# Kernel tuning notes

Hardware: AMD Instinct MI355X
Metric: run time of the kernel (lower is better)

The kernel has to match this reference:

```python
import jax, jax.numpy as jnp
import numpy as np

N, G, E, F, H = 100000, 32768, 1000000, 128, 128

def _mlp(x, w1, b1, w2, b2):
    # Linear -> SiLU -> Linear
    return jax.nn.silu(x @ w1 + b1) @ w2 + b2

def setup_inputs() -> dict:
    key = jax.random.key(0)
    ks = jax.random.split(key, 24)
    s = 0.02
    p = lambda k, shp: (jax.random.normal(k, shp, dtype=jnp.float32) * s)
    inp = {
        "node_features": jax.random.normal(ks[0], (N, F), dtype=jnp.float32),
        "node_pos": jax.random.normal(ks[1], (N, 3), dtype=jnp.float32),
        "grid_pos": jax.random.normal(ks[2], (G, 3), dtype=jnp.float32),
        "edge_index": jax.random.randint(ks[3], (2, E), 0, G, dtype=jnp.int64),
        "orientations": jax.random.normal(ks[4], (N, 3, 3), dtype=jnp.float32),
        # node_model
        "nw1": p(ks[5], (F, H)), "nb1": p(ks[6], (H,)),
        "nw2": p(ks[7], (H, H)), "nb2": p(ks[8], (H,)),
        # edge_model
        "ew1": p(ks[9], (6, H)), "eb1": p(ks[10], (H,)),
        "ew2": p(ks[11], (H, H)), "eb2": p(ks[12], (H,)),
        # message_model
        "mw1": p(ks[13], (2 * H, H)), "mb1": p(ks[14], (H,)),
        "mw2": p(ks[15], (H, H)), "mb2": p(ks[16], (H,)),
        # update_model
        "uw1": p(ks[17], (H, H)), "ub1": p(ks[18], (H,)),
        "uw2": p(ks[19], (H, H)), "ub2": p(ks[20], (H,)),
    }
    return inp

def reference(node_features, node_pos, grid_pos, edge_index, orientations,
              nw1, nb1, nw2, nb2, ew1, eb1, ew2, eb2,
              mw1, mb1, mw2, mb2, uw1, ub1, uw2, ub2):
    src, tgt = edge_index[0], edge_index[1]
    # node MLP on all points [N, H]
    node_h = _mlp(node_features, nw1, nb1, nw2, nb2)
    # per-edge geometry
    pos_src = node_pos[src]                     # [E, 3]
    rel_pos = grid_pos[tgt] - pos_src           # [E, 3]
    # bmm(rel_pos[e,1,3], orientations[src][e,3,3]) -> [E, 3]
    rot = jnp.einsum("ej,ejk->ek", rel_pos, orientations[src])
    edge_attr = jnp.concatenate([pos_src, rot], axis=-1)       # [E, 6]
    edge_h = _mlp(edge_attr, ew1, eb1, ew2, eb2)               # [E, H]
    msg_in = jnp.concatenate([node_h[src], edge_h], axis=-1)   # [E, 2H]
    msg = _mlp(msg_in, mw1, mb1, mw2, mb2)                     # [E, H]
    # scatter-mean to grid
    num_grid = grid_pos.shape[0]
    sums = jax.ops.segment_sum(msg, tgt, num_segments=num_grid)             # [G, H]
    counts = jax.ops.segment_sum(jnp.ones((msg.shape[0],), msg.dtype), tgt,
                                 num_segments=num_grid)
    grid_feat = sums / jnp.clip(counts, 1.0)[:, None]
    return _mlp(grid_feat, uw1, ub1, uw2, ub2)
```

## Files before the change

kernel.cpp:

```cpp
#include <hip/hip_runtime.h>

#define P 136

typedef __attribute__((ext_vector_type(8))) short short8;
typedef __attribute__((ext_vector_type(4))) float f32x4;

__device__ __forceinline__ unsigned short f2bf(float f) {
  union { float f; unsigned u; } v; v.f = f;
  unsigned u = v.u + 0x7fffu + ((v.u >> 16) & 1u);
  return (unsigned short)(u >> 16);
}
__device__ __forceinline__ float bf2f(unsigned short h) {
  union { unsigned u; float f; } v; v.u = ((unsigned)h) << 16;
  return v.f;
}
__device__ __forceinline__ unsigned pack2bf(float x, float y) {
  union { float f; unsigned u; } a, b; a.f = x; b.f = y;
  return __builtin_amdgcn_perm(b.u + 0x8000u, a.u + 0x8000u, 0x07060302u);
}
__device__ __forceinline__ float silu_f(float x) {
  float e = __expf(-x);
  return x * __builtin_amdgcn_rcpf(1.0f + e);
}

__device__ __forceinline__ void load_A128(const unsigned short* __restrict__ W,
                                          int m0w, int l16, int q, short8 a[2][4]) {
#pragma unroll
  for (int rt = 0; rt < 2; ++rt)
#pragma unroll
    for (int kt = 0; kt < 4; ++kt)
      a[rt][kt] = *(const short8*)&W[(m0w + rt * 16 + l16) * 128 + kt * 32 + q * 8];
}

template <int CT, bool INIT>
__device__ __forceinline__ void gemm_T(const short8 a[2][4],
                                       const unsigned short* sB,
                                       int l16, int q, f32x4 acc[2][CT]) {
  const f32x4 Z = (f32x4){0.f, 0.f, 0.f, 0.f};
#pragma unroll
  for (int kt = 0; kt < 4; ++kt)
#pragma unroll
    for (int ct = 0; ct < CT; ++ct) {
      short8 b = *(const short8*)&sB[(ct * 16 + l16) * P + kt * 32 + q * 8];
      f32x4 c0 = (INIT && kt == 0) ? Z : acc[0][ct];
      f32x4 c1 = (INIT && kt == 0) ? Z : acc[1][ct];
      acc[0][ct] = __builtin_amdgcn_mfma_f32_16x16x32_bf16(a[0][kt], b, c0, 0, 0, 0);
      acc[1][ct] = __builtin_amdgcn_mfma_f32_16x16x32_bf16(a[1][kt], b, c1, 0, 0, 0);
    }
}

template <bool SILU, int CT>
__device__ __forceinline__ void epilogue_T(const f32x4 acc[2][CT], const float* bias,
                                           unsigned short* sOut, int m0w, int l16,
                                           int q) {
#pragma unroll
  for (int rt = 0; rt < 2; ++rt) {
    int f0 = m0w + rt * 16 + q * 4;
    float4 bv = *(const float4*)&bias[f0];
#pragma unroll
    for (int ct = 0; ct < CT; ++ct) {
      float v0 = acc[rt][ct][0] + bv.x, v1 = acc[rt][ct][1] + bv.y;
      float v2 = acc[rt][ct][2] + bv.z, v3 = acc[rt][ct][3] + bv.w;
      if (SILU) { v0 = silu_f(v0); v1 = silu_f(v1); v2 = silu_f(v2); v3 = silu_f(v3); }
      uint2 w; w.x = pack2bf(v0, v1); w.y = pack2bf(v2, v3);
      *(uint2*)&sOut[(ct * 16 + l16) * P + f0] = w;
    }
  }
}

__global__ __launch_bounds__(256) void fold_hist_kernel(
    const float* __restrict__ nw1, const float* __restrict__ nw2,
    const float* __restrict__ nb2, const float* __restrict__ ew2,
    const float* __restrict__ eb2, const float* __restrict__ mw1,
    const float* __restrict__ mb1, const float* __restrict__ mw2,
    const float* __restrict__ uw1, const float* __restrict__ uw2,
    const float* __restrict__ ew1,
    unsigned short* __restrict__ nw1t, unsigned short* __restrict__ wnt,
    unsigned short* __restrict__ wct, unsigned short* __restrict__ mw2t,
    unsigned short* __restrict__ uw1t, unsigned short* __restrict__ uw2t,
    unsigned short* __restrict__ ew1t8,
    float* __restrict__ bn, float* __restrict__ bc,
    const int* __restrict__ eidx, int* __restrict__ hist, int E) {
  if (blockIdx.x >= 64) {
    int e0 = (blockIdx.x - 64) * 4096 + threadIdx.x * 16;
    if (e0 + 15 < E && (E & 3) == 0) {
      int4 t0 = *(const int4*)&eidx[E + e0];
      int4 t1 = *(const int4*)&eidx[E + e0 + 4];
      int4 t2 = *(const int4*)&eidx[E + e0 + 8];
      int4 t3 = *(const int4*)&eidx[E + e0 + 12];
      atomicAdd(&hist[t0.x], 1); atomicAdd(&hist[t0.y], 1);
      atomicAdd(&hist[t0.z], 1); atomicAdd(&hist[t0.w], 1);
      atomicAdd(&hist[t1.x], 1); atomicAdd(&hist[t1.y], 1);
      atomicAdd(&hist[t1.z], 1); atomicAdd(&hist[t1.w], 1);
      atomicAdd(&hist[t2.x], 1); atomicAdd(&hist[t2.y], 1);
      atomicAdd(&hist[t2.z], 1); atomicAdd(&hist[t2.w], 1);
      atomicAdd(&hist[t3.x], 1); atomicAdd(&hist[t3.y], 1);
      atomicAdd(&hist[t3.z], 1); atomicAdd(&hist[t3.w], 1);
    } else {
#pragma unroll
      for (int k = 0; k < 16; ++k) {
        int e = e0 + k;
        if (e < E) atomicAdd(&hist[eidx[E + e]], 1);
      }
    }
    return;
  }
  int b = blockIdx.x * 2 + (threadIdx.x >> 7);
  int t = threadIdx.x & 127;
  float accn = 0.f, accc = 0.f;
  for (int j = 0; j < 128; ++j) {
    accn += nw2[t * 128 + j] * mw1[j * 128 + b];
    accc += ew2[t * 128 + j] * mw1[(128 + j) * 128 + b];
  }
  wnt[b * 128 + t] = f2bf(accn);
  wct[b * 128 + t] = f2bf(accc);
  nw1t[b * 128 + t] = f2bf(nw1[t * 128 + b]);
  mw2t[b * 128 + t] = f2bf(mw2[t * 128 + b]);
  uw1t[b * 128 + t] = f2bf(uw1[t * 128 + b]);
  uw2t[b * 128 + t] = f2bf(uw2[t * 128 + b]);
  if (t < 8) ew1t8[b * 8 + t] = (t < 6) ? f2bf(ew1[t * 128 + b]) : (unsigned short)0;
  if (b == 0) {
    float sn = 0.f, sc = 0.f;
    for (int j = 0; j < 128; ++j) {
      sn += nb2[j] * mw1[j * 128 + t];
      sc += eb2[j] * mw1[(128 + j) * 128 + t];
    }
    bn[t] = sn;
    bc[t] = mb1[t] + sc;
  }
}

__global__ __launch_bounds__(1024) void scan_kernel(const int* __restrict__ hist,
                                                    int* __restrict__ cursor, int G) {
  __shared__ int s[1024];
  int tid = threadIdx.x;
  int per = (G + 1023) >> 10;
  int b0 = tid * per;
  bool vec = ((per & 3) == 0) && ((G & 3) == 0) && (b0 + per <= G);
  int sum = 0;
  if (vec) {
    for (int i = 0; i < per; i += 4) {
      int4 h = *(const int4*)&hist[b0 + i];
      sum += h.x + h.y + h.z + h.w;
    }
  } else {
    for (int i = 0; i < per; ++i)
      if (b0 + i < G) sum += hist[b0 + i];
  }
  s[tid] = sum;
  __syncthreads();
  for (int off = 1; off < 1024; off <<= 1) {
    int v = (tid >= off) ? s[tid - off] : 0;
    __syncthreads();
    s[tid] += v;
    __syncthreads();
  }
  int run = s[tid] - sum;
  if (vec) {
    for (int i = 0; i < per; i += 4) {
      int4 h = *(const int4*)&hist[b0 + i];
      int4 c;
      c.x = run;
      c.y = c.x + h.x;
      c.z = c.y + h.y;
      c.w = c.z + h.z;
      *(int4*)&cursor[b0 + i] = c;
      run = c.w + h.w;
    }
  } else {
    for (int i = 0; i < per; ++i)
      if (b0 + i < G) {
        cursor[b0 + i] = run;
        run += hist[b0 + i];
      }
  }
}

__global__ __launch_bounds__(256, 3) void scatter_node_kernel(
    const int* __restrict__ eidx, int* __restrict__ cursor,
    int2* __restrict__ st, int E, int nNode,
    const float* __restrict__ x, const float* __restrict__ nb1,
    const unsigned short* __restrict__ nw1t, const unsigned short* __restrict__ wnt,
    const float* __restrict__ bn, unsigned short* __restrict__ node_pre, int N) {
  __shared__ __align__(16) unsigned short s_x[128 * P];
  __shared__ __align__(16) float s_b1[128];
  __shared__ __align__(16) float s_bn[128];

  if (blockIdx.x >= (unsigned)nNode) {
    int e0 = (blockIdx.x - nNode) * 4096 + threadIdx.x * 16;
    if (e0 + 15 < E && (E & 3) == 0) {
      int4 sv[4], tv[4];
#pragma unroll
      for (int g = 0; g < 4; ++g) {
        sv[g] = *(const int4*)&eidx[e0 + g * 4];
        tv[g] = *(const int4*)&eidx[E + e0 + g * 4];
      }
      int pos[16];
#pragma unroll
      for (int g = 0; g < 4; ++g) {
        pos[g * 4 + 0] = atomicAdd(&cursor[tv[g].x], 1);
        pos[g * 4 + 1] = atomicAdd(&cursor[tv[g].y], 1);
        pos[g * 4 + 2] = atomicAdd(&cursor[tv[g].z], 1);
        pos[g * 4 + 3] = atomicAdd(&cursor[tv[g].w], 1);
      }
#pragma unroll
      for (int g = 0; g < 4; ++g) {
        st[pos[g * 4 + 0]] = make_int2(sv[g].x, tv[g].x);
        st[pos[g * 4 + 1]] = make_int2(sv[g].y, tv[g].y);
        st[pos[g * 4 + 2]] = make_int2(sv[g].z, tv[g].z);
        st[pos[g * 4 + 3]] = make_int2(sv[g].w, tv[g].w);
      }
    } else {
#pragma unroll
      for (int k = 0; k < 16; ++k) {
        int e = e0 + k;
        if (e < E) {
          int tg = eidx[E + e];
          int p = atomicAdd(&cursor[tg], 1);
          st[p] = make_int2(eidx[e], tg);
        }
      }
    }
    return;
  }

  int tid = threadIdx.x;
  long base = (long)blockIdx.x * 128;

#pragma unroll
  for (int i = 0; i < 16; ++i) {
    int flat = tid + i * 256;
    int row = flat >> 5;
    int c4 = (flat & 31) << 2;
    float4 v = make_float4(0.f, 0.f, 0.f, 0.f);
    if (base + row < N) v = *(const float4*)&x[(base + row) * 128 + c4];
    uint2 w; w.x = pack2bf(v.x, v.y); w.y = pack2bf(v.z, v.w);
    *(uint2*)&s_x[row * P + c4] = w;
  }
  if (tid < 128) { s_b1[tid] = nb1[tid]; s_bn[tid] = bn[tid]; }
  __syncthreads();

  int wave = tid >> 6, lane = tid & 63;
  int q = lane >> 4, l16 = lane & 15;
  int m0w = wave * 32;

  short8 a1[2][4];
  load_A128(nw1t, m0w, l16, q, a1);
  f32x4 acc[2][8];
  gemm_T<8, true>(a1, s_x, l16, q, acc);
  __syncthreads();
  epilogue_T<true, 8>(acc, s_b1, s_x, m0w, l16, q);
  __syncthreads();

  short8 a2[2][4];
  load_A128(wnt, m0w, l16, q, a2);
  gemm_T<8, true>(a2, s_x, l16, q, acc);

#pragma unroll
  for (int rt = 0; rt < 2; ++rt) {
    int f0 = m0w + rt * 16 + q * 4;
    float4 bv = *(const float4*)&s_bn[f0];
#pragma unroll
    for (int ct = 0; ct < 8; ++ct) {
      long n = base + ct * 16 + l16;
      if (n < N) {
        uint2 w;
        w.x = pack2bf(acc[rt][ct][0] + bv.x, acc[rt][ct][1] + bv.y);
        w.y = pack2bf(acc[rt][ct][2] + bv.z, acc[rt][ct][3] + bv.w);
        *(uint2*)&node_pre[n * 128 + f0] = w;
      }
    }
  }
}

__global__ __launch_bounds__(256, 4) void edge_kernel(
    const int2* __restrict__ st_sorted, const float* __restrict__ node_pos,
    const float* __restrict__ grid_pos, const float* __restrict__ ori,
    const unsigned short* __restrict__ ew1t8, const float* __restrict__ eb1,
    const unsigned short* __restrict__ wct, const float* __restrict__ bc,
    const unsigned short* __restrict__ node_pre, float* __restrict__ sums, int E) {
  __shared__ __align__(16) unsigned short s_h[128 * P];
  __shared__ int s_src[128];
  __shared__ int s_tgt[128];
  __shared__ __align__(16) float s_eb1[128];
  __shared__ __align__(16) float s_bc[128];

  int tid = threadIdx.x;
  int base = blockIdx.x * 128;

  if (tid < 128) {
    s_eb1[tid] = eb1[tid];
    s_bc[tid] = bc[tid];
    int eg = base + tid;
    int s = 0, tg = -1;
    float a0 = 0.f, a1 = 0.f, a2 = 0.f, a3 = 0.f, a4 = 0.f, a5 = 0.f;
    if (eg < E) {
      int2 st = st_sorted[eg];
      s = st.x; tg = st.y;
      float2 p01 = *(const float2*)&node_pos[s * 3];
      float pz = node_pos[s * 3 + 2];
      float2 g01 = *(const float2*)&grid_pos[tg * 3];
      float gz = grid_pos[tg * 3 + 2];
      float4 o0 = *(const float4*)&ori[(long)s * 9];
      float4 o1 = *(const float4*)&ori[(long)s * 9 + 4];
      float o8 = ori[(long)s * 9 + 8];
      float rx = g01.x - p01.x, ry = g01.y - p01.y, rz = gz - pz;
      a0 = p01.x; a1 = p01.y; a2 = pz;
      a3 = rx * o0.x + ry * o0.w + rz * o1.z;
      a4 = rx * o0.y + ry * o1.x + rz * o1.w;
      a5 = rx * o0.z + ry * o1.y + rz * o8;
    }
    s_src[tid] = s;
    s_tgt[tid] = tg;
    uint4 w0;
    w0.x = pack2bf(a0, a1); w0.y = pack2bf(a2, a3); w0.z = pack2bf(a4, a5); w0.w = 0u;
    *(uint4*)&s_h[tid * P] = w0;
  }

  int wave = tid >> 6, lane = tid & 63;
  int q = lane >> 4, l16 = lane & 15;
  int m0w = wave * 32;
  short8 z8 = (short8){0, 0, 0, 0, 0, 0, 0, 0};
  const f32x4 Z = (f32x4){0.f, 0.f, 0.f, 0.f};

  short8 ae0 = z8, ae1 = z8;
  if (q == 0) {
    ae0 = *(const short8*)&ew1t8[(m0w + l16) * 8];
    ae1 = *(const short8*)&ew1t8[(m0w + 16 + l16) * 8];
  }

  __syncthreads();

  short8 pre[8];
#pragma unroll
  for (int ct = 0; ct < 8; ++ct) {
    long srow = (long)s_src[ct * 16 + l16] * 128;
    pre[ct] = *(const short8*)&node_pre[srow + m0w + q * 8];
  }

  f32x4 acc[2][8];
#pragma unroll
  for (int ct = 0; ct < 8; ++ct) {
    short8 b = z8;
    if (q == 0) b = *(const short8*)&s_h[(ct * 16 + l16) * P];
    acc[0][ct] = __builtin_amdgcn_mfma_f32_16x16x32_bf16(ae0, b, Z, 0, 0, 0);
    acc[1][ct] = __builtin_amdgcn_mfma_f32_16x16x32_bf16(ae1, b, Z, 0, 0, 0);
  }
  __syncthreads();

  epilogue_T<true, 8>(acc, s_eb1, s_h, m0w, l16, q);

  short8 awc[2][4];
  load_A128(wct, m0w, l16, q, awc);

  __syncthreads();

  short8 aI_lo, aI_hi;
#pragma unroll
  for (int j = 0; j < 8; ++j) {
    aI_lo[j] = ((q * 8 + j) == l16) ? (short)0x3F80 : (short)0;
    aI_hi[j] = ((q * 8 + j) == (l16 + 16)) ? (short)0x3F80 : (short)0;
  }
#pragma unroll
  for (int ct = 0; ct < 8; ++ct) {
    acc[0][ct] = __builtin_amdgcn_mfma_f32_16x16x32_bf16(aI_lo, pre[ct], Z, 0, 0, 0);
    acc[1][ct] = __builtin_amdgcn_mfma_f32_16x16x32_bf16(aI_hi, pre[ct], Z, 0, 0, 0);
  }

  gemm_T<8, false>(awc, s_h, l16, q, acc);
  __syncthreads();

  epilogue_T<true, 8>(acc, s_bc, s_h, m0w, l16, q);
  __syncthreads();

  {
    int cq = tid & 31;
    int chunk = tid >> 5;
    int c0 = cq * 4;
    int row0 = chunk * 16;
    float v0 = 0.f, v1 = 0.f, v2 = 0.f, v3 = 0.f;
    int cur = s_tgt[row0];
    for (int r = 0; r < 16; ++r) {
      int row = row0 + r;
      int tg = s_tgt[row];
      if (tg != cur) {
        if (cur >= 0) {
          atomicAdd(&sums[(long)cur * 128 + c0], v0);
          atomicAdd(&sums[(long)cur * 128 + c0 + 1], v1);
          atomicAdd(&sums[(long)cur * 128 + c0 + 2], v2);
          atomicAdd(&sums[(long)cur * 128 + c0 + 3], v3);
        }
        v0 = 0.f; v1 = 0.f; v2 = 0.f; v3 = 0.f; cur = tg;
      }
      uint2 w = *(const uint2*)&s_h[row * P + c0];
      v0 += bf2f((unsigned short)w.x);
      v1 += bf2f((unsigned short)(w.x >> 16));
      v2 += bf2f((unsigned short)w.y);
      v3 += bf2f((unsigned short)(w.y >> 16));
    }
    if (cur >= 0) {
      atomicAdd(&sums[(long)cur * 128 + c0], v0);
      atomicAdd(&sums[(long)cur * 128 + c0 + 1], v1);
      atomicAdd(&sums[(long)cur * 128 + c0 + 2], v2);
      atomicAdd(&sums[(long)cur * 128 + c0 + 3], v3);
    }
  }
}

__global__ __launch_bounds__(256, 3) void grid_kernel(
    const float* __restrict__ sums, const int* __restrict__ hist,
    const float* __restrict__ mb2, const float* __restrict__ ub1,
    const float* __restrict__ ub2, const unsigned short* __restrict__ mw2t,
    const unsigned short* __restrict__ uw1t, const unsigned short* __restrict__ uw2t,
    float* __restrict__ out, int G) {
  __shared__ __align__(16) unsigned short s_x[32 * P];
  __shared__ __align__(16) float s_bm[128];
  __shared__ __align__(16) float s_b1[128];
  __shared__ __align__(16) float s_b2[128];
  int tid = threadIdx.x;
  long base = (long)blockIdx.x * 32;

#pragma unroll
  for (int i = 0; i < 4; ++i) {
    int flat = tid + i * 256;
    int row = flat >> 5;
    int c4 = (flat & 31) << 2;
    float4 v = make_float4(0.f, 0.f, 0.f, 0.f);
    float inv = 1.f;
    if (base + row < G) {
      v = *(const float4*)&sums[(base + row) * 128 + c4];
      int c = hist[base + row];
      inv = __builtin_amdgcn_rcpf((float)(c < 1 ? 1 : c));
    }
    uint2 w; w.x = pack2bf(v.x * inv, v.y * inv); w.y = pack2bf(v.z * inv, v.w * inv);
    *(uint2*)&s_x[row * P + c4] = w;
  }
  if (tid < 128) { s_bm[tid] = mb2[tid]; s_b1[tid] = ub1[tid]; s_b2[tid] = ub2[tid]; }
  __syncthreads();

  int wave = tid >> 6, lane = tid & 63;
  int q = lane >> 4, l16 = lane & 15;
  int m0w = wave * 32;

  f32x4 acc[2][2];
  short8 aw[2][4];

  load_A128(mw2t, m0w, l16, q, aw);
  gemm_T<2, true>(aw, s_x, l16, q, acc);
  __syncthreads();
  epilogue_T<false, 2>(acc, s_bm, s_x, m0w, l16, q);
  __syncthreads();

  load_A128(uw1t, m0w, l16, q, aw);
  gemm_T<2, true>(aw, s_x, l16, q, acc);
  __syncthreads();
  epilogue_T<true, 2>(acc, s_b1, s_x, m0w, l16, q);
  __syncthreads();

  load_A128(uw2t, m0w, l16, q, aw);
  gemm_T<2, true>(aw, s_x, l16, q, acc);

#pragma unroll
  for (int rt = 0; rt < 2; ++rt) {
    int f0 = m0w + rt * 16 + q * 4;
    float4 bv = *(const float4*)&s_b2[f0];
#pragma unroll
    for (int ct = 0; ct < 2; ++ct) {
      long g = base + ct * 16 + l16;
      if (g < G) {
        float4 o = make_float4(acc[rt][ct][0] + bv.x, acc[rt][ct][1] + bv.y,
                               acc[rt][ct][2] + bv.z, acc[rt][ct][3] + bv.w);
        *(float4*)&out[g * 128 + f0] = o;
      }
    }
  }
}

extern "C" void kernel_launch(void* const* d_in, const int* in_sizes, int n_in,
                              void* d_out, int out_size, void* d_ws, size_t ws_size,
                              hipStream_t stream) {
  const float* x    = (const float*)d_in[0];
  const float* npos = (const float*)d_in[1];
  const float* gpos = (const float*)d_in[2];
  const int*   eidx = (const int*)d_in[3];
  const float* ori  = (const float*)d_in[4];
  const float* nw1 = (const float*)d_in[5];
  const float* nb1 = (const float*)d_in[6];
  const float* nw2 = (const float*)d_in[7];
  const float* nb2 = (const float*)d_in[8];
  const float* ew1 = (const float*)d_in[9];
  const float* eb1 = (const float*)d_in[10];
  const float* ew2 = (const float*)d_in[11];
  const float* eb2 = (const float*)d_in[12];
  const float* mw1 = (const float*)d_in[13];
  const float* mb1 = (const float*)d_in[14];
  const float* mw2 = (const float*)d_in[15];
  const float* mb2 = (const float*)d_in[16];
  const float* uw1 = (const float*)d_in[17];
  const float* ub1 = (const float*)d_in[18];
  const float* uw2 = (const float*)d_in[19];
  const float* ub2 = (const float*)d_in[20];

  int N = in_sizes[0] / 128;
  int G = in_sizes[2] / 3;
  int E = in_sizes[3] / 2;

  char* ws = (char*)d_ws;
  size_t off = 0;
  float* sums = (float*)(ws + off);            off += (size_t)G * 128 * 4;
  int* hist = (int*)(ws + off);                off += (size_t)G * 4;
  int* cursor = (int*)(ws + off);              off += (size_t)G * 4;
  unsigned short* node_pre = (unsigned short*)(ws + off); off += (size_t)N * 128 * 2;
  off = (off + 255) & ~(size_t)255;
  unsigned short* w_nw1t = (unsigned short*)(ws + off); off += 128 * 128 * 2;
  unsigned short* w_wnt  = (unsigned short*)(ws + off); off += 128 * 128 * 2;
  unsigned short* w_wct  = (unsigned short*)(ws + off); off += 128 * 128 * 2;
  unsigned short* w_mw2t = (unsigned short*)(ws + off); off += 128 * 128 * 2;
  unsigned short* w_uw1t = (unsigned short*)(ws + off); off += 128 * 128 * 2;
  unsigned short* w_uw2t = (unsigned short*)(ws + off); off += 128 * 128 * 2;
  unsigned short* w_ew1t8 = (unsigned short*)(ws + off); off += 128 * 8 * 2;
  float* bn = (float*)(ws + off); off += 128 * 4;
  float* bc = (float*)(ws + off); off += 128 * 4;

  int2* st_sorted = (int2*)d_out;

  int nScat = (E + 4095) / 4096;
  int nNode = (N + 127) / 128;
  int nHist = (E + 4095) / 4096;

  hipMemsetAsync(sums, 0, ((size_t)G * 128 + G) * 4, stream);

  fold_hist_kernel<<<64 + nHist, 256, 0, stream>>>(
      nw1, nw2, nb2, ew2, eb2, mw1, mb1, mw2, uw1, uw2, ew1,
      w_nw1t, w_wnt, w_wct, w_mw2t, w_uw1t, w_uw2t, w_ew1t8, bn, bc,
      eidx, hist, E);
  scan_kernel<<<1, 1024, 0, stream>>>(hist, cursor, G);
  scatter_node_kernel<<<nNode + nScat, 256, 0, stream>>>(
      eidx, cursor, st_sorted, E, nNode,
      x, nb1, w_nw1t, w_wnt, bn, node_pre, N);
  edge_kernel<<<(E + 127) / 128, 256, 0, stream>>>(st_sorted, npos, gpos, ori,
                                                   w_ew1t8, eb1, w_wct, bc,
                                                   node_pre, sums, E);
  grid_kernel<<<(G + 31) / 32, 256, 0, stream>>>(sums, hist, mb2, ub1, ub2,
                                                 w_mw2t, w_uw1t, w_uw2t,
                                                 (float*)d_out, G);
}
```

Measured before the change: 465.4 us.

## Fold biases into MFMA accumulator init and rework edge scatter partitioning

Bias vectors are now loaded into registers and used as the initial MFMA accumulator, so the separate bias adds in every epilogue disappear. The edge kernel's launch bounds go from 4 to 3 blocks per SM, loosening register pressure. The segment-scatter phase now has each thread handle 2 columns over 32 rows instead of 4 columns over 16 rows, halving the atomic flushes per run boundary but lengthening each thread's serial loop.

```diff
diff --git a/kernel.cpp b/kernel.cpp
--- a/kernel.cpp
+++ b/kernel.cpp
@@ -32,35 +32,48 @@
       a[rt][kt] = *(const short8*)&W[(m0w + rt * 16 + l16) * 128 + kt * 32 + q * 8];
 }
 
-template <int CT, bool INIT>
-__device__ __forceinline__ void gemm_T(const short8 a[2][4],
-                                       const unsigned short* sB,
-                                       int l16, int q, f32x4 acc[2][CT]) {
-  const f32x4 Z = (f32x4){0.f, 0.f, 0.f, 0.f};
+template <int CT>
+__device__ __forceinline__ void gemm_T_init(const short8 a[2][4],
+                                            const unsigned short* sB,
+                                            int l16, int q, f32x4 acc[2][CT],
+                                            f32x4 c0i, f32x4 c1i) {
 #pragma unroll
   for (int kt = 0; kt < 4; ++kt)
 #pragma unroll
     for (int ct = 0; ct < CT; ++ct) {
       short8 b = *(const short8*)&sB[(ct * 16 + l16) * P + kt * 32 + q * 8];
-      f32x4 c0 = (INIT && kt == 0) ? Z : acc[0][ct];
-      f32x4 c1 = (INIT && kt == 0) ? Z : acc[1][ct];
+      f32x4 c0 = (kt == 0) ? c0i : acc[0][ct];
+      f32x4 c1 = (kt == 0) ? c1i : acc[1][ct];
       acc[0][ct] = __builtin_amdgcn_mfma_f32_16x16x32_bf16(a[0][kt], b, c0, 0, 0, 0);
       acc[1][ct] = __builtin_amdgcn_mfma_f32_16x16x32_bf16(a[1][kt], b, c1, 0, 0, 0);
     }
 }
 
+template <int CT>
+__device__ __forceinline__ void gemm_T_acc(const short8 a[2][4],
+                                           const unsigned short* sB,
+                                           int l16, int q, f32x4 acc[2][CT]) {
+#pragma unroll
+  for (int kt = 0; kt < 4; ++kt)
+#pragma unroll
+    for (int ct = 0; ct < CT; ++ct) {
+      short8 b = *(const short8*)&sB[(ct * 16 + l16) * P + kt * 32 + q * 8];
+      acc[0][ct] = __builtin_amdgcn_mfma_f32_16x16x32_bf16(a[0][kt], b, acc[0][ct], 0, 0, 0);
+      acc[1][ct] = __builtin_amdgcn_mfma_f32_16x16x32_bf16(a[1][kt], b, acc[1][ct], 0, 0, 0);
+    }
+}
+
 template <bool SILU, int CT>
-__device__ __forceinline__ void epilogue_T(const f32x4 acc[2][CT], const float* bias,
-                                           unsigned short* sOut, int m0w, int l16,
-                                           int q) {
+__device__ __forceinline__ void epilogue_nb(const f32x4 acc[2][CT],
+                                            unsigned short* sOut, int m0w, int l16,
+                                            int q) {
 #pragma unroll
   for (int rt = 0; rt < 2; ++rt) {
     int f0 = m0w + rt * 16 + q * 4;
-    float4 bv = *(const float4*)&bias[f0];
 #pragma unroll
     for (int ct = 0; ct < CT; ++ct) {
-      float v0 = acc[rt][ct][0] + bv.x, v1 = acc[rt][ct][1] + bv.y;
-      float v2 = acc[rt][ct][2] + bv.z, v3 = acc[rt][ct][3] + bv.w;
+      float v0 = acc[rt][ct][0], v1 = acc[rt][ct][1];
+      float v2 = acc[rt][ct][2], v3 = acc[rt][ct][3];
       if (SILU) { v0 = silu_f(v0); v1 = silu_f(v1); v2 = silu_f(v2); v3 = silu_f(v3); }
       uint2 w; w.x = pack2bf(v0, v1); w.y = pack2bf(v2, v3);
       *(uint2*)&sOut[(ct * 16 + l16) * P + f0] = w;
@@ -244,36 +257,40 @@
   int q = lane >> 4, l16 = lane & 15;
   int m0w = wave * 32;
 
+  f32x4 b1_0 = *(const f32x4*)&s_b1[m0w + q * 4];
+  f32x4 b1_1 = *(const f32x4*)&s_b1[m0w + 16 + q * 4];
+
   short8 a1[2][4];
   load_A128(nw1t, m0w, l16, q, a1);
   f32x4 acc[2][8];
-  gemm_T<8, true>(a1, s_x, l16, q, acc);
-  __syncthreads();
-  epilogue_T<true, 8>(acc, s_b1, s_x, m0w, l16, q);
-  __syncthreads();
-
+  gemm_T_init<8>(a1, s_x, l16, q, acc, b1_0, b1_1);
+  __syncthreads();
+  epilogue_nb<true, 8>(acc, s_x, m0w, l16, q);
+  __syncthreads();
+
+  f32x4 bn_0 = *(const f32x4*)&s_bn[m0w + q * 4];
+  f32x4 bn_1 = *(const f32x4*)&s_bn[m0w + 16 + q * 4];
   short8 a2[2][4];
   load_A128(wnt, m0w, l16, q, a2);
-  gemm_T<8, true>(a2, s_x, l16, q, acc);
+  gemm_T_init<8>(a2, s_x, l16, q, acc, bn_0, bn_1);
 
 #pragma unroll
   for (int rt = 0; rt < 2; ++rt) {
     int f0 = m0w + rt * 16 + q * 4;
-    float4 bv = *(const float4*)&s_bn[f0];
 #pragma unroll
     for (int ct = 0; ct < 8; ++ct) {
       long n = base + ct * 16 + l16;
       if (n < N) {
         uint2 w;
-        w.x = pack2bf(acc[rt][ct][0] + bv.x, acc[rt][ct][1] + bv.y);
-        w.y = pack2bf(acc[rt][ct][2] + bv.z, acc[rt][ct][3] + bv.w);
+        w.x = pack2bf(acc[rt][ct][0], acc[rt][ct][1]);
+        w.y = pack2bf(acc[rt][ct][2], acc[rt][ct][3]);
         *(uint2*)&node_pre[n * 128 + f0] = w;
       }
     }
   }
 }
 
-__global__ __launch_bounds__(256, 4) void edge_kernel(
+__global__ __launch_bounds__(256, 3) void edge_kernel(
     const int2* __restrict__ st_sorted, const float* __restrict__ node_pos,
     const float* __restrict__ grid_pos, const float* __restrict__ ori,
     const unsigned short* __restrict__ ew1t8, const float* __restrict__ eb1,
@@ -321,7 +338,6 @@
   int q = lane >> 4, l16 = lane & 15;
   int m0w = wave * 32;
   short8 z8 = (short8){0, 0, 0, 0, 0, 0, 0, 0};
-  const f32x4 Z = (f32x4){0.f, 0.f, 0.f, 0.f};
 
   short8 ae0 = z8, ae1 = z8;
   if (q == 0) {
@@ -338,23 +354,28 @@
     pre[ct] = *(const short8*)&node_pre[srow + m0w + q * 8];
   }
 
+  f32x4 be0 = *(const f32x4*)&s_eb1[m0w + q * 4];
+  f32x4 be1 = *(const f32x4*)&s_eb1[m0w + 16 + q * 4];
+
   f32x4 acc[2][8];
 #pragma unroll
   for (int ct = 0; ct < 8; ++ct) {
     short8 b = z8;
     if (q == 0) b = *(const short8*)&s_h[(ct * 16 + l16) * P];
-    acc[0][ct] = __builtin_amdgcn_mfma_f32_16x16x32_bf16(ae0, b, Z, 0, 0, 0);
-    acc[1][ct] = __builtin_amdgcn_mfma_f32_16x16x32_bf16(ae1, b, Z, 0, 0, 0);
-  }
-  __syncthreads();
-
-  epilogue_T<true, 8>(acc, s_eb1, s_h, m0w, l16, q);
+    acc[0][ct] = __builtin_amdgcn_mfma_f32_16x16x32_bf16(ae0, b, be0, 0, 0, 0);
+    acc[1][ct] = __builtin_amdgcn_mfma_f32_16x16x32_bf16(ae1, b, be1, 0, 0, 0);
+  }
+  __syncthreads();
+
+  epilogue_nb<true, 8>(acc, s_h, m0w, l16, q);
 
   short8 awc[2][4];
   load_A128(wct, m0w, l16, q, awc);
 
   __syncthreads();
 
+  f32x4 bc0 = *(const f32x4*)&s_bc[m0w + q * 4];
+  f32x4 bc1 = *(const f32x4*)&s_bc[m0w + 16 + q * 4];
   short8 aI_lo, aI_hi;
 #pragma unroll
   for (int j = 0; j < 8; ++j) {
@@ -363,46 +384,40 @@
   }
 #pragma unroll
   for (int ct = 0; ct < 8; ++ct) {
-    acc[0][ct] = __builtin_amdgcn_mfma_f32_16x16x32_bf16(aI_lo, pre[ct], Z, 0, 0, 0);
-    acc[1][ct] = __builtin_amdgcn_mfma_f32_16x16x32_bf16(aI_hi, pre[ct], Z, 0, 0, 0);
-  }
-
-  gemm_T<8, false>(awc, s_h, l16, q, acc);
-  __syncthreads();
-
-  epilogue_T<true, 8>(acc, s_bc, s_h, m0w, l16, q);
+    acc[0][ct] = __builtin_amdgcn_mfma_f32_16x16x32_bf16(aI_lo, pre[ct], bc0, 0, 0, 0);
+    acc[1][ct] = __builtin_amdgcn_mfma_f32_16x16x32_bf16(aI_hi, pre[ct], bc1, 0, 0, 0);
+  }
+
+  gemm_T_acc<8>(awc, s_h, l16, q, acc);
+  __syncthreads();
+
+  epilogue_nb<true, 8>(acc, s_h, m0w, l16, q);
   __syncthreads();
 
   {
-    int cq = tid & 31;
-    int chunk = tid >> 5;
-    int c0 = cq * 4;
-    int row0 = chunk * 16;
-    float v0 = 0.f, v1 = 0.f, v2 = 0.f, v3 = 0.f;
+    int cp = tid & 63;
+    int chunk = tid >> 6;
+    int c0 = cp * 2;
+    int row0 = chunk * 32;
+    float v0 = 0.f, v1 = 0.f;
     int cur = s_tgt[row0];
-    for (int r = 0; r < 16; ++r) {
+    for (int r = 0; r < 32; ++r) {
       int row = row0 + r;
       int tg = s_tgt[row];
       if (tg != cur) {
         if (cur >= 0) {
           atomicAdd(&sums[(long)cur * 128 + c0], v0);
           atomicAdd(&sums[(long)cur * 128 + c0 + 1], v1);
-          atomicAdd(&sums[(long)cur * 128 + c0 + 2], v2);
-          atomicAdd(&sums[(long)cur * 128 + c0 + 3], v3);
         }
-        v0 = 0.f; v1 = 0.f; v2 = 0.f; v3 = 0.f; cur = tg;
-      }
-      uint2 w = *(const uint2*)&s_h[row * P + c0];
-      v0 += bf2f((unsigned short)w.x);
-      v1 += bf2f((unsigned short)(w.x >> 16));
-      v2 += bf2f((unsigned short)w.y);
-      v3 += bf2f((unsigned short)(w.y >> 16));
+        v0 = 0.f; v1 = 0.f; cur = tg;
+      }
+      unsigned w = *(const unsigned*)&s_h[row * P + c0];
+      v0 += bf2f((unsigned short)w);
+      v1 += bf2f((unsigned short)(w >> 16));
     }
     if (cur >= 0) {
       atomicAdd(&sums[(long)cur * 128 + c0], v0);
       atomicAdd(&sums[(long)cur * 128 + c0 + 1], v1);
-      atomicAdd(&sums[(long)cur * 128 + c0 + 2], v2);
-      atomicAdd(&sums[(long)cur * 128 + c0 + 3], v3);
     }
   }
 }
@@ -445,31 +460,37 @@
   f32x4 acc[2][2];
   short8 aw[2][4];
 
+  f32x4 bm0 = *(const f32x4*)&s_bm[m0w + q * 4];
+  f32x4 bm1 = *(const f32x4*)&s_bm[m0w + 16 + q * 4];
+  f32x4 b10 = *(const f32x4*)&s_b1[m0w + q * 4];
+  f32x4 b11 = *(const f32x4*)&s_b1[m0w + 16 + q * 4];
+  f32x4 b20 = *(const f32x4*)&s_b2[m0w + q * 4];
+  f32x4 b21 = *(const f32x4*)&s_b2[m0w + 16 + q * 4];
+
   load_A128(mw2t, m0w, l16, q, aw);
-  gemm_T<2, true>(aw, s_x, l16, q, acc);
-  __syncthreads();
-  epilogue_T<false, 2>(acc, s_bm, s_x, m0w, l16, q);
+  gemm_T_init<2>(aw, s_x, l16, q, acc, bm0, bm1);
+  __syncthreads();
+  epilogue_nb<false, 2>(acc, s_x, m0w, l16, q);
   __syncthreads();
 
   load_A128(uw1t, m0w, l16, q, aw);
-  gemm_T<2, true>(aw, s_x, l16, q, acc);
-  __syncthreads();
-  epilogue_T<true, 2>(acc, s_b1, s_x, m0w, l16, q);
+  gemm_T_init<2>(aw, s_x, l16, q, acc, b10, b11);
+  __syncthreads();
+  epilogue_nb<true, 2>(acc, s_x, m0w, l16, q);
   __syncthreads();
 
   load_A128(uw2t, m0w, l16, q, aw);
-  gemm_T<2, true>(aw, s_x, l16, q, acc);
+  gemm_T_init<2>(aw, s_x, l16, q, acc, b20, b21);
 
 #pragma unroll
   for (int rt = 0; rt < 2; ++rt) {
     int f0 = m0w + rt * 16 + q * 4;
-    float4 bv = *(const float4*)&s_b2[f0];
 #pragma unroll
     for (int ct = 0; ct < 2; ++ct) {
       long g = base + ct * 16 + l16;
       if (g < G) {
-        float4 o = make_float4(acc[rt][ct][0] + bv.x, acc[rt][ct][1] + bv.y,
-                               acc[rt][ct][2] + bv.z, acc[rt][ct][3] + bv.w);
+        float4 o = make_float4(acc[rt][ct][0], acc[rt][ct][1],
+                               acc[rt][ct][2], acc[rt][ct][3]);
         *(float4*)&out[g * 128 + f0] = o;
       }
     }
```

After: 407.6 us. 1.14x faster.
